# Kernel tuning notes

Measured on AMD Instinct MI355X. Metric: run time of the kernel, lower is better.

Reference implementation:

```python
import jax, jax.numpy as jnp
import numpy as np

B, S, E = 2, 2048, 2048
H, HKV, D = 32, 8, 64  # n_heads, n_kv_heads, head_dim


def _rope(x, cos, sin):
    # x: [B,S,h,D]; cos/sin: [1,S,1,D//2]. Complex rotate on (even,odd) pairs.
    xp = x.reshape(*x.shape[:-1], D // 2, 2)
    x0, x1 = xp[..., 0], xp[..., 1]
    r0 = x0 * cos - x1 * sin
    r1 = x0 * sin + x1 * cos
    return jnp.stack([r0, r1], axis=-1).reshape(x.shape)


def setup_inputs() -> dict:
    key = jax.random.key(0)
    ks = jax.random.split(key, 8)
    sc = 0.02
    # real RoPE frequencies (theta=10000) for realism
    inv = 1.0 / (10000.0 ** (np.arange(0, D, 2, dtype=np.float32) / D))
    t = np.arange(S, dtype=np.float32)
    ang = np.outer(t, inv)  # [S, D/2]
    return {
        "x": jax.random.normal(ks[0], (B, S, E), jnp.float32),
        "start_pos": 0,
        "freqs_cos": jnp.asarray(np.cos(ang))[None, :, None, :],
        "freqs_sin": jnp.asarray(np.sin(ang))[None, :, None, :],
        "wq": jax.random.normal(ks[1], (E, H * D), jnp.float32) * sc,
        "wk": jax.random.normal(ks[2], (E, HKV * D), jnp.float32) * sc,
        "wv": jax.random.normal(ks[3], (E, HKV * D), jnp.float32) * sc,
        "out_w": jax.random.normal(ks[4], (H * D, E), jnp.float32) * sc,
        "out_b": jnp.zeros((E,), jnp.float32),
        "k_cache": jnp.zeros((B, S, HKV, D), jnp.float32),
        "v_cache": jnp.zeros((B, S, HKV, D), jnp.float32),
    }


def reference(x, start_pos, freqs_cos, freqs_sin, wq, wk, wv, out_w, out_b, k_cache, v_cache):
    b, s, _ = x.shape
    q = (x @ wq).reshape(b, s, H, D)
    k = (x @ wk).reshape(b, s, HKV, D)
    v = (x @ wv).reshape(b, s, HKV, D)
    q = _rope(q, freqs_cos[:, :s], freqs_sin[:, :s])
    k = _rope(k, freqs_cos[:, :s], freqs_sin[:, :s])
    # KV-cache append (torch code detaches before writing)
    k_cache = jax.lax.dynamic_update_slice(k_cache, jax.lax.stop_gradient(k), (0, start_pos, 0, 0))
    v_cache = jax.lax.dynamic_update_slice(v_cache, jax.lax.stop_gradient(v), (0, start_pos, 0, 0))
    keys = k_cache[:b, : start_pos + s]    # [b, T, HKV, D]
    values = v_cache[:b, : start_pos + s]
    g = H // HKV
    if g > 1:  # GQA head repeat
        keys = jnp.repeat(keys, g, axis=2)     # [b, T, H, D]
        values = jnp.repeat(values, g, axis=2)
    scores = jnp.einsum("bqhd,bkhd->bhqk", q, keys) / jnp.sqrt(jnp.float32(D))
    att = jax.nn.softmax(scores, axis=-1)  # NOTE: source applies no causal mask
    o = jnp.einsum("bhqk,bkhd->bqhd", att, values).reshape(b, s, H * D)
    return o @ out_w + out_b
```

## Files before the change

kernel.cpp:

```cpp
#include <hip/hip_runtime.h>
#include <math.h>

#define B_    2
#define S_    2048
#define E_    2048
#define H_    32
#define HKV_  8
#define D_    64

typedef __bf16 bf16x8 __attribute__((ext_vector_type(8)));
typedef __bf16 bf16x4 __attribute__((ext_vector_type(4)));
typedef float  f32x4  __attribute__((ext_vector_type(4)));

#define GPTR(x) ((const __attribute__((address_space(1))) void*)(x))
#define LPTR(x) ((__attribute__((address_space(3))) void*)(x))

__global__ __launch_bounds__(256) void convert_kernel(
    const float* __restrict__ in, __bf16* __restrict__ out, int n8)
{
    const int i = blockIdx.x * 256 + threadIdx.x;
    if (i >= n8) return;
    const float4 a = ((const float4*)in)[i * 2];
    const float4 b = ((const float4*)in)[i * 2 + 1];
    bf16x8 o;
    o[0] = (__bf16)a.x; o[1] = (__bf16)a.y; o[2] = (__bf16)a.z; o[3] = (__bf16)a.w;
    o[4] = (__bf16)b.x; o[5] = (__bf16)b.y; o[6] = (__bf16)b.z; o[7] = (__bf16)b.w;
    ((bf16x8*)out)[i] = o;
}

__global__ __launch_bounds__(256) void transpose_convert_kernel(
    const float* __restrict__ in, __bf16* __restrict__ out, int K, int N)
{
    __shared__ float tile[32][33];
    const int k0 = blockIdx.y * 32, n0 = blockIdx.x * 32;
    const int r  = threadIdx.x >> 3;
    const int c4 = (threadIdx.x & 7) * 4;
    const float4 v = *(const float4*)&in[(size_t)(k0 + r) * N + n0 + c4];
    tile[r][c4 + 0] = v.x; tile[r][c4 + 1] = v.y;
    tile[r][c4 + 2] = v.z; tile[r][c4 + 3] = v.w;
    __syncthreads();
    ushort4 o;
    __bf16 h0 = (__bf16)tile[c4 + 0][r]; o.x = __builtin_bit_cast(unsigned short, h0);
    __bf16 h1 = (__bf16)tile[c4 + 1][r]; o.y = __builtin_bit_cast(unsigned short, h1);
    __bf16 h2 = (__bf16)tile[c4 + 2][r]; o.z = __builtin_bit_cast(unsigned short, h2);
    __bf16 h3 = (__bf16)tile[c4 + 3][r]; o.w = __builtin_bit_cast(unsigned short, h3);
    *(ushort4*)&out[(size_t)(n0 + r) * K + k0 + c4] = o;
}

__device__ __forceinline__ void gemm_mfma_body(
    const __bf16* __restrict__ A, const __bf16* __restrict__ Bt,
    int m0, int n0, int K, __bf16* sA, __bf16* sB, f32x4 acc[4][4])
{
    const int t    = threadIdx.x;
    const int w    = t >> 6;
    const int lane = t & 63;
    const int col  = lane & 15;
    const int quad = lane >> 4;
    const int wrow = (w >> 1) * 64;
    const int wcol = (w & 1) * 64;

    const int row0 = t >> 3;
    const int c0   = t & 7;

    for (int k0 = 0; k0 < K; k0 += 64) {
#pragma unroll
        for (int it = 0; it < 4; ++it) {
            const int row  = it * 32 + row0;
            const int csrc = c0 ^ (row & 7);
            __builtin_amdgcn_global_load_lds(
                GPTR(A + (size_t)(m0 + row) * K + k0 + csrc * 8),
                LPTR(sA + (it * 256 + t) * 8), 16, 0, 0);
        }
#pragma unroll
        for (int it = 0; it < 4; ++it) {
            const int row  = it * 32 + row0;
            const int csrc = c0 ^ (row & 7);
            __builtin_amdgcn_global_load_lds(
                GPTR(Bt + (size_t)(n0 + row) * K + k0 + csrc * 8),
                LPTR(sB + (it * 256 + t) * 8), 16, 0, 0);
        }
        __syncthreads();

#pragma unroll
        for (int kk = 0; kk < 2; ++kk) {
            bf16x8 af[4], bfr[4];
#pragma unroll
            for (int i = 0; i < 4; ++i) {
                const int m = wrow + i * 16 + col;
                af[i] = *(const bf16x8*)&sA[m * 64 + (((kk * 4 + quad) ^ (m & 7)) * 8)];
            }
#pragma unroll
            for (int j = 0; j < 4; ++j) {
                const int n = wcol + j * 16 + col;
                bfr[j] = *(const bf16x8*)&sB[n * 64 + (((kk * 4 + quad) ^ (n & 7)) * 8)];
            }
#pragma unroll
            for (int i = 0; i < 4; ++i)
#pragma unroll
                for (int j = 0; j < 4; ++j)
                    acc[i][j] = __builtin_amdgcn_mfma_f32_16x16x32_bf16(
                        af[i], bfr[j], acc[i][j], 0, 0, 0);
        }
        __syncthreads();
    }
}

__global__ __launch_bounds__(256) void gemm_qkv_kernel(
    const __bf16* __restrict__ xb, const __bf16* __restrict__ wT,
    __bf16* __restrict__ qb, __bf16* __restrict__ kb, __bf16* __restrict__ vb)
{
    __shared__ __bf16 sA[128 * 64];
    __shared__ __bf16 sB[128 * 64];
    f32x4 acc[4][4];
#pragma unroll
    for (int i = 0; i < 4; ++i)
#pragma unroll
        for (int j = 0; j < 4; ++j) acc[i][j] = (f32x4){0.f, 0.f, 0.f, 0.f};

    const int bx = blockIdx.x;
    const int m0 = blockIdx.y * 128;
    gemm_mfma_body(xb, wT, m0, bx * 128, E_, sA, sB, acc);

    __bf16* Cp; int ldc, nb;
    if (bx < 16)      { Cp = qb; ldc = H_ * D_;   nb = bx * 128; }
    else if (bx < 20) { Cp = kb; ldc = HKV_ * D_; nb = (bx - 16) * 128; }
    else              { Cp = vb; ldc = HKV_ * D_; nb = (bx - 20) * 128; }

    const int lane = threadIdx.x & 63;
    const int col  = lane & 15;
    const int quad = lane >> 4;
    const int wrow = ((threadIdx.x >> 6) >> 1) * 64;
    const int wcol = ((threadIdx.x >> 6) & 1) * 64;
#pragma unroll
    for (int i = 0; i < 4; ++i)
#pragma unroll
        for (int j = 0; j < 4; ++j)
#pragma unroll
            for (int r = 0; r < 4; ++r) {
                const int m = m0 + wrow + i * 16 + quad * 4 + r;
                const int n = nb + wcol + j * 16 + col;
                Cp[(size_t)m * ldc + n] = (__bf16)acc[i][j][r];
            }
}

__global__ __launch_bounds__(256) void gemm_out_kernel(
    const __bf16* __restrict__ ob, const __bf16* __restrict__ woT,
    const float* __restrict__ bias, float* __restrict__ out)
{
    __shared__ __bf16 sA[128 * 64];
    __shared__ __bf16 sB[128 * 64];
    f32x4 acc[4][4];
#pragma unroll
    for (int i = 0; i < 4; ++i)
#pragma unroll
        for (int j = 0; j < 4; ++j) acc[i][j] = (f32x4){0.f, 0.f, 0.f, 0.f};

    const int m0 = blockIdx.y * 128;
    const int n0 = blockIdx.x * 128;
    gemm_mfma_body(ob, woT, m0, n0, H_ * D_, sA, sB, acc);

    const int lane = threadIdx.x & 63;
    const int col  = lane & 15;
    const int quad = lane >> 4;
    const int wrow = ((threadIdx.x >> 6) >> 1) * 64;
    const int wcol = ((threadIdx.x >> 6) & 1) * 64;
#pragma unroll
    for (int i = 0; i < 4; ++i)
#pragma unroll
        for (int j = 0; j < 4; ++j)
#pragma unroll
            for (int r = 0; r < 4; ++r) {
                const int m = m0 + wrow + i * 16 + quad * 4 + r;
                const int n = n0 + wcol + j * 16 + col;
                out[(size_t)m * E_ + n] = acc[i][j][r] + bias[n];
            }
}

__global__ __launch_bounds__(256) void rope_kernel(
    __bf16* __restrict__ p, const float* __restrict__ fc,
    const float* __restrict__ fs, int nh, int npairs)
{
    const int i = blockIdx.x * 256 + threadIdx.x;
    if (i >= npairs) return;
    const int pair = i & 31;
    const int row  = i >> 5;
    const int s    = (row / nh) % S_;
    const unsigned int v = ((const unsigned int*)p)[i];
    const float x0 = (float)__builtin_bit_cast(__bf16, (unsigned short)(v & 0xffff));
    const float x1 = (float)__builtin_bit_cast(__bf16, (unsigned short)(v >> 16));
    const float c  = fc[s * 32 + pair];
    const float sn = fs[s * 32 + pair];
    const __bf16 r0 = (__bf16)(x0 * c - x1 * sn);
    const __bf16 r1 = (__bf16)(x0 * sn + x1 * c);
    ((unsigned int*)p)[i] =
        ((unsigned int)__builtin_bit_cast(unsigned short, r1) << 16) |
        (unsigned int)__builtin_bit_cast(unsigned short, r0);
}

__global__ __launch_bounds__(256, 2) void attn_kernel(
    const __bf16* __restrict__ qw, const __bf16* __restrict__ kw,
    const __bf16* __restrict__ vw, __bf16* __restrict__ ow)
{
    __shared__ __bf16 sK [64][72];
    __shared__ __bf16 sVT[64][72];
    __shared__ __bf16 sP [4][64][72];

    const int t    = threadIdx.x;
    const int w    = t >> 6;
    const int lane = t & 63;
    const int col  = lane & 15;
    const int quad = lane >> 4;

    const int bh  = blockIdx.y;
    const int b   = bh >> 5;
    const int h   = bh & 31;
    const int kvh = h >> 2;
    const int q0w = blockIdx.x * 256 + w * 64;

    const int KSTR = HKV_ * D_;

    bf16x8 bQ[4][2];
#pragma unroll
    for (int qf = 0; qf < 4; ++qf) {
        const __bf16* qrow = qw + (((size_t)b * S_ + q0w + qf * 16 + col) * H_ + h) * D_;
        bQ[qf][0] = ((const bf16x8*)qrow)[quad];
        bQ[qf][1] = ((const bf16x8*)qrow)[4 + quad];
    }

    f32x4 O[4][4];
#pragma unroll
    for (int qf = 0; qf < 4; ++qf)
#pragma unroll
        for (int dt = 0; dt < 4; ++dt) O[qf][dt] = (f32x4){0.f, 0.f, 0.f, 0.f};
    float lr[4] = {0.f, 0.f, 0.f, 0.f};

    const __bf16* kbase = kw + ((size_t)b * S_ * HKV_ + kvh) * D_;
    const __bf16* vbase = vw + ((size_t)b * S_ * HKV_ + kvh) * D_;

    const int kkey = t >> 2;
    const int kd   = (t & 3) * 16;
    const int vkp  = (t & 31) * 2;
    const int vdg  = (t >> 5) * 4;

    for (int j0 = 0; j0 < S_; j0 += 64) {
        {
            const __bf16* kr = kbase + (size_t)(j0 + kkey) * KSTR + kd;
            *(bf16x8*)&sK[kkey][kd]     = ((const bf16x8*)kr)[0];
            *(bf16x8*)&sK[kkey][kd + 8] = ((const bf16x8*)kr)[1];
        }
#pragma unroll
        for (int r = 0; r < 64; r += 32) {
            const __bf16* v0 = vbase + (size_t)(j0 + vkp) * KSTR + vdg + r;
            const __bf16* v1 = v0 + KSTR;
            const ushort4 ua = *(const ushort4*)v0;
            const ushort4 uc = *(const ushort4*)v1;
            *(unsigned int*)&sVT[vdg + r + 0][vkp] = ((unsigned int)uc.x << 16) | ua.x;
            *(unsigned int*)&sVT[vdg + r + 1][vkp] = ((unsigned int)uc.y << 16) | ua.y;
            *(unsigned int*)&sVT[vdg + r + 2][vkp] = ((unsigned int)uc.z << 16) | ua.z;
            *(unsigned int*)&sVT[vdg + r + 3][vkp] = ((unsigned int)uc.w << 16) | ua.w;
        }
        __syncthreads();

#pragma unroll
        for (int st = 0; st < 4; ++st) {
            const bf16x8 aK0 = *(const bf16x8*)&sK[st * 16 + col][quad * 8];
            const bf16x8 aK1 = *(const bf16x8*)&sK[st * 16 + col][32 + quad * 8];
#pragma unroll
            for (int qf = 0; qf < 4; ++qf) {
                f32x4 sc = (f32x4){0.f, 0.f, 0.f, 0.f};
                sc = __builtin_amdgcn_mfma_f32_16x16x32_bf16(aK0, bQ[qf][0], sc, 0, 0, 0);
                sc = __builtin_amdgcn_mfma_f32_16x16x32_bf16(aK1, bQ[qf][1], sc, 0, 0, 0);
                bf16x4 pk;
                float psum = 0.f;
#pragma unroll
                for (int r = 0; r < 4; ++r) {
                    const float p = __expf(sc[r] * 0.125f);
                    psum += p;
                    pk[r] = (__bf16)p;
                }
                lr[qf] += psum;
                *(bf16x4*)&sP[w][qf * 16 + col][st * 16 + quad * 4] = pk;
            }
        }

        bf16x8 vbf[4][2];
#pragma unroll
        for (int dt = 0; dt < 4; ++dt) {
            vbf[dt][0] = *(const bf16x8*)&sVT[dt * 16 + col][quad * 8];
            vbf[dt][1] = *(const bf16x8*)&sVT[dt * 16 + col][32 + quad * 8];
        }
#pragma unroll
        for (int qf = 0; qf < 4; ++qf) {
            const bf16x8 pa0 = *(const bf16x8*)&sP[w][qf * 16 + col][quad * 8];
            const bf16x8 pa1 = *(const bf16x8*)&sP[w][qf * 16 + col][32 + quad * 8];
#pragma unroll
            for (int dt = 0; dt < 4; ++dt) {
                O[qf][dt] = __builtin_amdgcn_mfma_f32_16x16x32_bf16(pa0, vbf[dt][0], O[qf][dt], 0, 0, 0);
                O[qf][dt] = __builtin_amdgcn_mfma_f32_16x16x32_bf16(pa1, vbf[dt][1], O[qf][dt], 0, 0, 0);
            }
        }
        __syncthreads();
    }

#pragma unroll
    for (int qf = 0; qf < 4; ++qf) {
        lr[qf] += __shfl_xor(lr[qf], 16);
        lr[qf] += __shfl_xor(lr[qf], 32);
    }

#pragma unroll
    for (int qf = 0; qf < 4; ++qf)
#pragma unroll
        for (int r = 0; r < 4; ++r) {
            const float lv  = __shfl(lr[qf], quad * 4 + r);
            const float inv = 1.f / lv;
            const int   qr  = q0w + qf * 16 + quad * 4 + r;
            __bf16* orow = ow + (((size_t)b * S_ + qr) * H_ + h) * D_;
#pragma unroll
            for (int dt = 0; dt < 4; ++dt)
                orow[dt * 16 + col] = (__bf16)(O[qf][dt][r] * inv);
        }
}

extern "C" void kernel_launch(void* const* d_in, const int* in_sizes, int n_in,
                              void* d_out, int out_size, void* d_ws, size_t ws_size,
                              hipStream_t stream)
{
    const float* x  = (const float*)d_in[0];
    const float* fc = (const float*)d_in[2];
    const float* fs = (const float*)d_in[3];
    const float* wq = (const float*)d_in[4];
    const float* wk = (const float*)d_in[5];
    const float* wv = (const float*)d_in[6];
    const float* wo = (const float*)d_in[7];
    const float* obias = (const float*)d_in[8];
    float* out = (float*)d_out;

    __bf16* ws  = (__bf16*)d_ws;
    __bf16* xb  = ws;
    __bf16* wT  = xb  + (size_t)4096 * 2048;
    __bf16* woT = wT  + (size_t)3072 * 2048;
    __bf16* qb  = woT + (size_t)2048 * 2048;
    __bf16* kb  = qb  + (size_t)B_ * S_ * H_ * D_;
    __bf16* vb  = kb  + (size_t)B_ * S_ * HKV_ * D_;
    __bf16* obf = vb  + (size_t)B_ * S_ * HKV_ * D_;

    convert_kernel<<<4096, 256, 0, stream>>>(x, xb, 4096 * 2048 / 8);
    transpose_convert_kernel<<<dim3(64, 64), 256, 0, stream>>>(wq, wT, E_, 2048);
    transpose_convert_kernel<<<dim3(16, 64), 256, 0, stream>>>(wk, wT + (size_t)2048 * 2048, E_, 512);
    transpose_convert_kernel<<<dim3(16, 64), 256, 0, stream>>>(wv, wT + (size_t)2560 * 2048, E_, 512);
    transpose_convert_kernel<<<dim3(64, 64), 256, 0, stream>>>(wo, woT, H_ * D_, E_);

    gemm_qkv_kernel<<<dim3(24, 32), 256, 0, stream>>>(xb, wT, qb, kb, vb);

    rope_kernel<<<(B_ * S_ * H_ * 32 + 255) / 256, 256, 0, stream>>>(
        qb, fc, fs, H_, B_ * S_ * H_ * 32);
    rope_kernel<<<(B_ * S_ * HKV_ * 32 + 255) / 256, 256, 0, stream>>>(
        kb, fc, fs, HKV_, B_ * S_ * HKV_ * 32);

    attn_kernel<<<dim3(S_ / 256, B_ * H_), 256, 0, stream>>>(qb, kb, vb, obf);

    gemm_out_kernel<<<dim3(16, 32), 256, 0, stream>>>(obf, woT, obias, out);
}
```

Before: 383.8 us.

## Rewrite attention with 32x32 MFMA, register-resident P, double-buffered K/V

```diff
diff --git a/kernel.cpp b/kernel.cpp
--- a/kernel.cpp
+++ b/kernel.cpp
@@ -11,9 +11,14 @@
 typedef __bf16 bf16x8 __attribute__((ext_vector_type(8)));
 typedef __bf16 bf16x4 __attribute__((ext_vector_type(4)));
 typedef float  f32x4  __attribute__((ext_vector_type(4)));
+typedef float  f32x16 __attribute__((ext_vector_type(16)));
+typedef unsigned int u32x2 __attribute__((ext_vector_type(2)));
+typedef unsigned int u32x4 __attribute__((ext_vector_type(4)));
 
 #define GPTR(x) ((const __attribute__((address_space(1))) void*)(x))
 #define LPTR(x) ((__attribute__((address_space(3))) void*)(x))
+
+#define QK_SCALE_LOG2E 0.18033688011112042f
 
 __global__ __launch_bounds__(256) void convert_kernel(
     const float* __restrict__ in, __bf16* __restrict__ out, int n8)
@@ -126,6 +131,8 @@
     else if (bx < 20) { Cp = kb; ldc = HKV_ * D_; nb = (bx - 16) * 128; }
     else              { Cp = vb; ldc = HKV_ * D_; nb = (bx - 20) * 128; }
 
+    const float qsc = (bx < 16) ? QK_SCALE_LOG2E : 1.0f;
+
     const int lane = threadIdx.x & 63;
     const int col  = lane & 15;
     const int quad = lane >> 4;
@@ -139,7 +146,7 @@
             for (int r = 0; r < 4; ++r) {
                 const int m = m0 + wrow + i * 16 + quad * 4 + r;
                 const int n = nb + wcol + j * 16 + col;
-                Cp[(size_t)m * ldc + n] = (__bf16)acc[i][j][r];
+                Cp[(size_t)m * ldc + n] = (__bf16)(acc[i][j][r] * qsc);
             }
 }
 
@@ -197,129 +204,161 @@
         (unsigned int)__builtin_bit_cast(unsigned short, r0);
 }
 
-__global__ __launch_bounds__(256, 2) void attn_kernel(
+struct StageRegs {
+    bf16x8  k0, k1;
+    ushort4 va0, vc0, va1, vc1;
+};
+
+__device__ __forceinline__ void stage_load(
+    StageRegs& r, const __bf16* kbase, const __bf16* vbase, int j0,
+    int kkey, int kd, int vkp, int vdg)
+{
+    const int KSTR = HKV_ * D_;
+    const __bf16* kr = kbase + (size_t)(j0 + kkey) * KSTR + kd;
+    r.k0 = ((const bf16x8*)kr)[0];
+    r.k1 = ((const bf16x8*)kr)[1];
+    const __bf16* v0 = vbase + (size_t)(j0 + vkp) * KSTR + vdg;
+    r.va0 = *(const ushort4*)(v0);
+    r.vc0 = *(const ushort4*)(v0 + KSTR);
+    r.va1 = *(const ushort4*)(v0 + 32);
+    r.vc1 = *(const ushort4*)(v0 + KSTR + 32);
+}
+
+__device__ __forceinline__ void stage_write(
+    const StageRegs& r, __bf16 (*sK)[72], __bf16 (*sVT)[72],
+    int kkey, int kd, int vkp, int vdg)
+{
+    *(bf16x8*)&sK[kkey][kd]     = r.k0;
+    *(bf16x8*)&sK[kkey][kd + 8] = r.k1;
+    *(unsigned int*)&sVT[vdg + 0][vkp]      = ((unsigned)r.vc0.x << 16) | r.va0.x;
+    *(unsigned int*)&sVT[vdg + 1][vkp]      = ((unsigned)r.vc0.y << 16) | r.va0.y;
+    *(unsigned int*)&sVT[vdg + 2][vkp]      = ((unsigned)r.vc0.z << 16) | r.va0.z;
+    *(unsigned int*)&sVT[vdg + 3][vkp]      = ((unsigned)r.vc0.w << 16) | r.va0.w;
+    *(unsigned int*)&sVT[vdg + 32 + 0][vkp] = ((unsigned)r.vc1.x << 16) | r.va1.x;
+    *(unsigned int*)&sVT[vdg + 32 + 1][vkp] = ((unsigned)r.vc1.y << 16) | r.va1.y;
+    *(unsigned int*)&sVT[vdg + 32 + 2][vkp] = ((unsigned)r.vc1.z << 16) | r.va1.z;
+    *(unsigned int*)&sVT[vdg + 32 + 3][vkp] = ((unsigned)r.vc1.w << 16) | r.va1.w;
+}
+
+__device__ __forceinline__ bf16x8 pack_pa(const f32x16& p, int i0)
+{
+    unsigned a0, a1, a2, a3;
+    asm("v_cvt_pk_bf16_f32 %0, %1, %2" : "=v"(a0) : "v"(p[i0 + 0]), "v"(p[i0 + 1]));
+    asm("v_cvt_pk_bf16_f32 %0, %1, %2" : "=v"(a1) : "v"(p[i0 + 2]), "v"(p[i0 + 3]));
+    asm("v_cvt_pk_bf16_f32 %0, %1, %2" : "=v"(a2) : "v"(p[i0 + 4]), "v"(p[i0 + 5]));
+    asm("v_cvt_pk_bf16_f32 %0, %1, %2" : "=v"(a3) : "v"(p[i0 + 6]), "v"(p[i0 + 7]));
+    const u32x2 s02 = __builtin_amdgcn_permlane32_swap(a0, a2, false, false);
+    const u32x2 s13 = __builtin_amdgcn_permlane32_swap(a1, a3, false, false);
+    return __builtin_bit_cast(bf16x8, (u32x4){s02[0], s13[0], s02[1], s13[1]});
+}
+
+__device__ __forceinline__ void attn_tile(
+    const __bf16 (*sK)[72], const __bf16 (*sVT)[72],
+    const bf16x8* bQ, int lq, int hi,
+    f32x16& O0, f32x16& O1, float& lsum)
+{
+    bf16x8 pa[4];
+#pragma unroll
+    for (int kb = 0; kb < 2; ++kb) {
+        f32x16 p;
+#pragma unroll
+        for (int i = 0; i < 16; ++i) p[i] = 0.f;
+        __builtin_amdgcn_s_setprio(1);
+#pragma unroll
+        for (int ks = 0; ks < 4; ++ks) {
+            const bf16x8 aK = *(const bf16x8*)&sK[kb * 32 + lq][ks * 16 + hi * 8];
+            p = __builtin_amdgcn_mfma_f32_32x32x16_bf16(aK, bQ[ks], p, 0, 0, 0);
+        }
+        __builtin_amdgcn_s_setprio(0);
+        float ps = 0.f;
+#pragma unroll
+        for (int i = 0; i < 16; ++i) {
+            p[i] = __builtin_amdgcn_exp2f(p[i]);
+            ps += p[i];
+        }
+        lsum += ps;
+        pa[kb * 2]     = pack_pa(p, 0);
+        pa[kb * 2 + 1] = pack_pa(p, 8);
+    }
+    __builtin_amdgcn_s_setprio(1);
+#pragma unroll
+    for (int ks = 0; ks < 4; ++ks) {
+        const bf16x8 vb0 = *(const bf16x8*)&sVT[lq][ks * 16 + hi * 8];
+        const bf16x8 vb1 = *(const bf16x8*)&sVT[32 + lq][ks * 16 + hi * 8];
+        O0 = __builtin_amdgcn_mfma_f32_32x32x16_bf16(pa[ks], vb0, O0, 0, 0, 0);
+        O1 = __builtin_amdgcn_mfma_f32_32x32x16_bf16(pa[ks], vb1, O1, 0, 0, 0);
+    }
+    __builtin_amdgcn_s_setprio(0);
+}
+
+__global__ __launch_bounds__(256, 3) void attn_kernel(
     const __bf16* __restrict__ qw, const __bf16* __restrict__ kw,
     const __bf16* __restrict__ vw, __bf16* __restrict__ ow)
 {
-    __shared__ __bf16 sK [64][72];
-    __shared__ __bf16 sVT[64][72];
-    __shared__ __bf16 sP [4][64][72];
+    __shared__ __bf16 sK0[64][72], sVT0[64][72];
+    __shared__ __bf16 sK1[64][72], sVT1[64][72];
 
     const int t    = threadIdx.x;
+    const int lane = t & 63;
     const int w    = t >> 6;
-    const int lane = t & 63;
-    const int col  = lane & 15;
-    const int quad = lane >> 4;
+    const int lq   = lane & 31;
+    const int hi   = lane >> 5;
 
     const int bh  = blockIdx.y;
     const int b   = bh >> 5;
     const int h   = bh & 31;
     const int kvh = h >> 2;
-    const int q0w = blockIdx.x * 256 + w * 64;
-
-    const int KSTR = HKV_ * D_;
-
-    bf16x8 bQ[4][2];
-#pragma unroll
-    for (int qf = 0; qf < 4; ++qf) {
-        const __bf16* qrow = qw + (((size_t)b * S_ + q0w + qf * 16 + col) * H_ + h) * D_;
-        bQ[qf][0] = ((const bf16x8*)qrow)[quad];
-        bQ[qf][1] = ((const bf16x8*)qrow)[4 + quad];
-    }
-
-    f32x4 O[4][4];
-#pragma unroll
-    for (int qf = 0; qf < 4; ++qf)
-#pragma unroll
-        for (int dt = 0; dt < 4; ++dt) O[qf][dt] = (f32x4){0.f, 0.f, 0.f, 0.f};
-    float lr[4] = {0.f, 0.f, 0.f, 0.f};
+    const int q0  = blockIdx.x * 128 + w * 32;
+
+    bf16x8 bQ[4];
+    {
+        const __bf16* qrow = qw + (((size_t)b * S_ + q0 + lq) * H_ + h) * D_;
+#pragma unroll
+        for (int ks = 0; ks < 4; ++ks)
+            bQ[ks] = *(const bf16x8*)(qrow + ks * 16 + hi * 8);
+    }
+
+    f32x16 O0, O1;
+#pragma unroll
+    for (int i = 0; i < 16; ++i) { O0[i] = 0.f; O1[i] = 0.f; }
+    float lsum = 0.f;
 
     const __bf16* kbase = kw + ((size_t)b * S_ * HKV_ + kvh) * D_;
     const __bf16* vbase = vw + ((size_t)b * S_ * HKV_ + kvh) * D_;
-
-    const int kkey = t >> 2;
-    const int kd   = (t & 3) * 16;
-    const int vkp  = (t & 31) * 2;
-    const int vdg  = (t >> 5) * 4;
-
-    for (int j0 = 0; j0 < S_; j0 += 64) {
-        {
-            const __bf16* kr = kbase + (size_t)(j0 + kkey) * KSTR + kd;
-            *(bf16x8*)&sK[kkey][kd]     = ((const bf16x8*)kr)[0];
-            *(bf16x8*)&sK[kkey][kd + 8] = ((const bf16x8*)kr)[1];
-        }
-#pragma unroll
-        for (int r = 0; r < 64; r += 32) {
-            const __bf16* v0 = vbase + (size_t)(j0 + vkp) * KSTR + vdg + r;
-            const __bf16* v1 = v0 + KSTR;
-            const ushort4 ua = *(const ushort4*)v0;
-            const ushort4 uc = *(const ushort4*)v1;
-            *(unsigned int*)&sVT[vdg + r + 0][vkp] = ((unsigned int)uc.x << 16) | ua.x;
-            *(unsigned int*)&sVT[vdg + r + 1][vkp] = ((unsigned int)uc.y << 16) | ua.y;
-            *(unsigned int*)&sVT[vdg + r + 2][vkp] = ((unsigned int)uc.z << 16) | ua.z;
-            *(unsigned int*)&sVT[vdg + r + 3][vkp] = ((unsigned int)uc.w << 16) | ua.w;
-        }
+    const int kkey = t >> 2,        kd  = (t & 3) * 16;
+    const int vkp  = (t & 31) * 2,  vdg = (t >> 5) * 4;
+
+    StageRegs sr;
+    stage_load(sr, kbase, vbase, 0, kkey, kd, vkp, vdg);
+    stage_write(sr, sK0, sVT0, kkey, kd, vkp, vdg);
+    __syncthreads();
+
+#pragma unroll 1
+    for (int j0 = 0; j0 < S_; j0 += 128) {
+        StageRegs nx;
+        stage_load(nx, kbase, vbase, j0 + 64, kkey, kd, vkp, vdg);
+        attn_tile(sK0, sVT0, bQ, lq, hi, O0, O1, lsum);
+        stage_write(nx, sK1, sVT1, kkey, kd, vkp, vdg);
         __syncthreads();
-
-#pragma unroll
-        for (int st = 0; st < 4; ++st) {
-            const bf16x8 aK0 = *(const bf16x8*)&sK[st * 16 + col][quad * 8];
-            const bf16x8 aK1 = *(const bf16x8*)&sK[st * 16 + col][32 + quad * 8];
-#pragma unroll
-            for (int qf = 0; qf < 4; ++qf) {
-                f32x4 sc = (f32x4){0.f, 0.f, 0.f, 0.f};
-                sc = __builtin_amdgcn_mfma_f32_16x16x32_bf16(aK0, bQ[qf][0], sc, 0, 0, 0);
-                sc = __builtin_amdgcn_mfma_f32_16x16x32_bf16(aK1, bQ[qf][1], sc, 0, 0, 0);
-                bf16x4 pk;
-                float psum = 0.f;
-#pragma unroll
-                for (int r = 0; r < 4; ++r) {
-                    const float p = __expf(sc[r] * 0.125f);
-                    psum += p;
-                    pk[r] = (__bf16)p;
-                }
-                lr[qf] += psum;
-                *(bf16x4*)&sP[w][qf * 16 + col][st * 16 + quad * 4] = pk;
-            }
-        }
-
-        bf16x8 vbf[4][2];
-#pragma unroll
-        for (int dt = 0; dt < 4; ++dt) {
-            vbf[dt][0] = *(const bf16x8*)&sVT[dt * 16 + col][quad * 8];
-            vbf[dt][1] = *(const bf16x8*)&sVT[dt * 16 + col][32 + quad * 8];
-        }
-#pragma unroll
-        for (int qf = 0; qf < 4; ++qf) {
-            const bf16x8 pa0 = *(const bf16x8*)&sP[w][qf * 16 + col][quad * 8];
-            const bf16x8 pa1 = *(const bf16x8*)&sP[w][qf * 16 + col][32 + quad * 8];
-#pragma unroll
-            for (int dt = 0; dt < 4; ++dt) {
-                O[qf][dt] = __builtin_amdgcn_mfma_f32_16x16x32_bf16(pa0, vbf[dt][0], O[qf][dt], 0, 0, 0);
-                O[qf][dt] = __builtin_amdgcn_mfma_f32_16x16x32_bf16(pa1, vbf[dt][1], O[qf][dt], 0, 0, 0);
-            }
-        }
+        if (j0 + 128 < S_)
+            stage_load(nx, kbase, vbase, j0 + 128, kkey, kd, vkp, vdg);
+        attn_tile(sK1, sVT1, bQ, lq, hi, O0, O1, lsum);
+        if (j0 + 128 < S_)
+            stage_write(nx, sK0, sVT0, kkey, kd, vkp, vdg);
         __syncthreads();
     }
 
-#pragma unroll
-    for (int qf = 0; qf < 4; ++qf) {
-        lr[qf] += __shfl_xor(lr[qf], 16);
-        lr[qf] += __shfl_xor(lr[qf], 32);
-    }
-
-#pragma unroll
-    for (int qf = 0; qf < 4; ++qf)
-#pragma unroll
-        for (int r = 0; r < 4; ++r) {
-            const float lv  = __shfl(lr[qf], quad * 4 + r);
-            const float inv = 1.f / lv;
-            const int   qr  = q0w + qf * 16 + quad * 4 + r;
-            __bf16* orow = ow + (((size_t)b * S_ + qr) * H_ + h) * D_;
-#pragma unroll
-            for (int dt = 0; dt < 4; ++dt)
-                orow[dt * 16 + col] = (__bf16)(O[qf][dt][r] * inv);
-        }
+    lsum += __shfl_xor(lsum, 32);
+    const float inv = 1.0f / lsum;
+
+#pragma unroll
+    for (int r = 0; r < 16; ++r) {
+        const int   qr = (r & 3) + 8 * (r >> 2) + 4 * hi;
+        const float li = __shfl(inv, qr);
+        __bf16* orow = ow + (((size_t)b * S_ + q0 + qr) * H_ + h) * D_;
+        orow[lq]      = (__bf16)(O0[r] * li);
+        orow[32 + lq] = (__bf16)(O1[r] * li);
+    }
 }
 
 extern "C" void kernel_launch(void* const* d_in, const int* in_sizes, int n_in,
@@ -358,7 +397,7 @@
     rope_kernel<<<(B_ * S_ * HKV_ * 32 + 255) / 256, 256, 0, stream>>>(
         kb, fc, fs, HKV_, B_ * S_ * HKV_ * 32);
 
-    attn_kernel<<<dim3(S_ / 256, B_ * H_), 256, 0, stream>>>(qb, kb, vb, obf);
+    attn_kernel<<<dim3(S_ / 128, B_ * H_), 256, 0, stream>>>(qb, kb, vb, obf);
 
     gemm_out_kernel<<<dim3(16, 32), 256, 0, stream>>>(obf, woT, obias, out);
 }
```

New measurement: 375.8 us. 1.02x faster.
